# Kernel optimization log

Hardware: AMD Instinct MI355X
Metric: run time of the kernel (lower is better)

## Reference

```python
import jax, jax.numpy as jnp
import numpy as np

FIX_SCALE = np.array([[0.,0.,0.],[1.,0.,0.],[0.,1.,0.],[0.,0.,1.],[-1.,0.,0.],[0.,-1.,0.]], dtype=np.float32)
NUM_HEADS = 8
ATTN_DIMS = 512
HEAD_DIMS = ATTN_DIMS // NUM_HEADS
NUM_LEARN = 6
SIG_CLAMP = 9.21  # safe_sigmoid clamp


def quat_to_rotmat(q):
    # q: [G,4] (w,x,y,z), normalized -> [G,3,3]
    q = q / jnp.linalg.norm(q, axis=-1, keepdims=True)
    w, x, y, z = q[..., 0], q[..., 1], q[..., 2], q[..., 3]
    r0 = jnp.stack([1 - 2*(y*y + z*z), 2*(x*y - w*z), 2*(x*z + w*y)], -1)
    r1 = jnp.stack([2*(x*y + w*z), 1 - 2*(x*x + z*z), 2*(y*z - w*x)], -1)
    r2 = jnp.stack([2*(x*z - w*y), 2*(y*z + w*x), 1 - 2*(x*x + y*y)], -1)
    return jnp.stack([r0, r1, r2], -2)


def bilinear_sample(fm, gx, gy):
    # fm: [C,H,W]; gx,gy: [...] in [-1,1]; align_corners=False, zero padding
    C, H, W = fm.shape
    x = (gx + 1.0) * (W * 0.5) - 0.5
    y = (gy + 1.0) * (H * 0.5) - 0.5
    x0 = jnp.floor(x); y0 = jnp.floor(y)
    wx1 = x - x0; wx0 = 1.0 - wx1
    wy1 = y - y0; wy0 = 1.0 - wy1

    def gather(xf, yf):
        xi = xf.astype(jnp.int32); yi = yf.astype(jnp.int32)
        valid = (xi >= 0) & (xi < W) & (yi >= 0) & (yi < H)
        xi = jnp.clip(xi, 0, W - 1); yi = jnp.clip(yi, 0, H - 1)
        return fm[:, yi, xi] * valid[None].astype(fm.dtype)  # [C, ...]

    out = (gather(x0, y0) * (wx0 * wy0)[None]
           + gather(x0 + 1, y0) * (wx1 * wy0)[None]
           + gather(x0, y0 + 1) * (wx0 * wy1)[None]
           + gather(x0 + 1, y0 + 1) * (wx1 * wy1)[None])
    return jnp.moveaxis(out, 0, -1)  # [..., C]


def setup_inputs() -> dict:
    key = jax.random.key(0)
    ks = jax.random.split(key, 16)
    G, BS, GFD = 8192, 1, 32
    means = jax.random.uniform(ks[0], (G, 3), minval=-1.0, maxval=1.0)
    means = means.at[:, 2].add(3.0)  # push in front of camera
    scales = jax.random.uniform(ks[1], (G, 3), minval=0.01, maxval=0.1)
    rotations = jax.random.normal(ks[2], (G, 4))
    features = jax.random.normal(ks[3], (BS, G, 3, GFD))
    transforms = jnp.tile(jnp.eye(4)[None], (G, 1, 1)) + 0.01 * jax.random.normal(ks[4], (G, 4, 4))
    f = 64.0
    proj = jnp.array([[f, 0., 32., 0.], [0., f, 32., 0.], [0., 0., 1., 0.], [0., 0., 0., 1.]], dtype=jnp.float32)
    projection = jnp.tile(proj[None], (BS, 1, 1))
    image_features = jax.random.normal(ks[5], (BS, 256, 64, 64))
    s = lambda d: 1.0 / np.sqrt(d)
    Wq = jax.random.normal(ks[6], (GFD, ATTN_DIMS)) * s(GFD)
    Wk = jax.random.normal(ks[7], (ATTN_DIMS, 256)) * s(256)
    Wv = jax.random.normal(ks[8], (ATTN_DIMS, 256)) * s(256)
    W_off = jax.random.normal(ks[9], (HEAD_DIMS + 3, NUM_LEARN * 3)) * s(HEAD_DIMS + 3)
    b_off = jnp.zeros((NUM_LEARN * 3,))
    Wout = jax.random.normal(ks[10], (ATTN_DIMS, GFD)) * s(ATTN_DIMS)
    b_out = jnp.zeros((GFD,))
    return {"means": means, "scales": scales, "rotations": rotations, "features": features,
            "transforms": transforms, "projection": projection, "image_features": image_features,
            "Wq": Wq, "Wk": Wk, "Wv": Wv, "W_off": W_off, "b_off": b_off, "Wout": Wout, "b_out": b_out}


def reference(means, scales, rotations, features, transforms, projection, image_features,
              Wq, Wk, Wv, W_off, b_off, Wout, b_out):
    G = means.shape[0]
    bs = features.shape[0]
    H, HD = NUM_HEADS, HEAD_DIMS
    h_img, w_img = image_features.shape[-2:]

    # queries: [bs,G,3,attn] -> [bs,H,G,3,hd]
    q_full = jnp.einsum('bgtf,fa->bgta', features, Wq)
    q = q_full.reshape(bs, G, 3, H, HD).transpose(0, 3, 1, 2, 4)

    # transform means to world space with per-gaussian 4x4
    homo = jnp.concatenate([means, jnp.ones((G, 1), means.dtype)], -1)  # [G,4]
    means_w = jnp.einsum('gij,gj->gi', transforms, homo)[:, :3]  # [G,3]

    # OffsetNet: per-head learnable offsets from (world mean, token-mean query)
    q_mean = q.mean(axis=3)  # [bs,H,G,hd]
    m_b = jnp.broadcast_to(means_w[None, None], (bs, H, G, 3))
    off_in = jnp.concatenate([m_b, q_mean], -1)  # [bs,H,G,hd+3]
    learnable = jax.nn.sigmoid(jnp.clip(off_in @ W_off + b_off, -SIG_CLAMP, SIG_CLAMP))
    learnable = learnable.reshape(bs, H, G, NUM_LEARN, 3) - 0.5
    fix = jnp.broadcast_to(jnp.asarray(FIX_SCALE)[None, None, None], (bs, H, G, FIX_SCALE.shape[0], 3))
    scale_all = jnp.concatenate([fix, learnable], axis=-2)  # [bs,H,G,K,3]
    K = scale_all.shape[-2]

    offset_pts = scale_all * scales[None, None, :, None, :]
    RT = jnp.swapaxes(quat_to_rotmat(rotations), -1, -2)  # [G,3,3]
    offset_pts = jnp.einsum('gij,bhgkj->bhgki', RT, offset_pts) + means_w[None, None, :, None, :]

    # project to 2D, normalize to [0,1), then to grid coords [-1,1]
    pts4 = jnp.concatenate([offset_pts, jnp.ones_like(offset_pts[..., :1])], -1)
    p = jnp.einsum('bij,bhgkj->bhgki', projection, pts4)
    p2 = p[..., :2] / jnp.clip(p[..., 2:3], 1e-5)
    wh = jnp.array([w_img, h_img], dtype=p2.dtype)
    pnorm = jnp.clip(p2 / wh, 0.0, 0.9999)
    grid = 2.0 * pnorm - 1.0  # [bs,H,G,K,2]

    # key/value maps via 1x1 conv, split into per-head channel groups
    kmap = jnp.einsum('ac,bchw->bahw', Wk, image_features).reshape(bs, H, HD, h_img, w_img)
    vmap_ = jnp.einsum('ac,bchw->bahw', Wv, image_features).reshape(bs, H, HD, h_img, w_img)

    sample_bh = jax.vmap(jax.vmap(bilinear_sample, in_axes=(0, 0, 0)), in_axes=(0, 0, 0))
    k_s = sample_bh(kmap, grid[..., 0], grid[..., 1])   # [bs,H,G,K,hd]
    v_s = sample_bh(vmap_, grid[..., 0], grid[..., 1])  # [bs,H,G,K,hd]

    scale = HD ** -0.5
    scores = jnp.einsum('bhgid,bhgkd->bhgik', q, k_s) * scale
    attn = jax.nn.softmax(scores, axis=-1)
    out = jnp.einsum('bhgik,bhgkd->bhgid', attn, v_s)  # [bs,H,G,3,hd]
    out = out.transpose(0, 2, 3, 1, 4).reshape(bs, G, 3, H * HD)  # b g i (h d)
    out = out @ Wout + b_out
    return out + features
```

## Files before the change

kernel.cpp:

```cpp
#include <hip/hip_runtime.h>
#include <hip/hip_bf16.h>
#include <hip/hip_fp16.h>

typedef _Float16 half2v __attribute__((ext_vector_type(2)));
typedef _Float16 half8v __attribute__((ext_vector_type(8)));
typedef __attribute__((ext_vector_type(4))) float float4v;

__device__ __forceinline__ half2v u2h(unsigned u) { return __builtin_bit_cast(half2v, u); }
__device__ __forceinline__ unsigned h2u(half2v h) { return __builtin_bit_cast(unsigned, h); }
__device__ __forceinline__ unsigned short f2hu(float f) {
    _Float16 h = (_Float16)f; return __builtin_bit_cast(unsigned short, h);
}
__device__ __forceinline__ unsigned packh(float lo, float hi) {
    half2v h; h[0] = (_Float16)lo; h[1] = (_Float16)hi; return h2u(h);
}
__device__ __forceinline__ void ld8h(const unsigned short* p, float* f) {
    uint4 u = *(const uint4*)p;
    half2v h0 = u2h(u.x), h1 = u2h(u.y), h2 = u2h(u.z), h3 = u2h(u.w);
    f[0] = (float)h0[0]; f[1] = (float)h0[1]; f[2] = (float)h1[0]; f[3] = (float)h1[1];
    f[4] = (float)h2[0]; f[5] = (float)h2[1]; f[6] = (float)h3[0]; f[7] = (float)h3[1];
}

__global__ __launch_bounds__(256) void wcomb_kernel(
    const float* __restrict__ Wq, const float* __restrict__ W_off,
    const float* __restrict__ b_off, float* __restrict__ Wall)
{
    const int gid = blockIdx.x * 256 + threadIdx.x;
    if (gid >= 36 * 144) return;
    const int j = gid / 144, c = gid - j * 144;
    const int h = c / 18, l = c - h * 18;
    float v;
    if (j < 3) {
        v = W_off[j * 18 + l];
    } else if (j < 35) {
        const int f = j - 3;
        const float* wq = Wq + (size_t)f * 512 + h * 64;
        float s = 0.f;
#pragma unroll
        for (int d = 0; d < 64; d++) s += wq[d] * W_off[(size_t)(3 + d) * 18 + l];
        v = s;
    } else {
        v = b_off[l];
    }
    Wall[gid] = v;
}

__global__ __launch_bounds__(256) void offmlp_kernel(
    const float* __restrict__ means, const float* __restrict__ transforms,
    const float* __restrict__ features, const float* __restrict__ Wall,
    float* __restrict__ lrn_all)
{
    __shared__ float Wc[36][144];
    __shared__ float A[16][38];
    const int tid = threadIdx.x;
    const int g0 = blockIdx.x * 16;

    for (int i = tid; i < 36 * 144; i += 256) Wc[i / 144][i - (i / 144) * 144] = Wall[i];
    {
        const int gi = tid >> 4, lane = tid & 15;
        const int g = g0 + gi;
        const float* fb = features + (size_t)g * 96 + lane * 2;
        float2 t0 = *(const float2*)(fb);
        float2 t1 = *(const float2*)(fb + 32);
        float2 t2 = *(const float2*)(fb + 64);
        A[gi][3 + lane * 2]     = (t0.x + t1.x + t2.x) * (1.f / 3.f);
        A[gi][3 + lane * 2 + 1] = (t0.y + t1.y + t2.y) * (1.f / 3.f);
        if (lane < 3) {
            const float* T = transforms + (size_t)g * 16 + lane * 4;
            float m0 = means[(size_t)g * 3];
            float m1 = means[(size_t)g * 3 + 1];
            float m2 = means[(size_t)g * 3 + 2];
            A[gi][lane] = T[0] * m0 + T[1] * m1 + T[2] * m2 + T[3];
        } else if (lane == 3) {
            A[gi][35] = 1.f;
        }
    }
    __syncthreads();

#pragma unroll
    for (int k = 0; k < 9; k++) {
        int oi = tid + k * 256;
        int gi = oi / 144, c = oi - gi * 144;
        float s = 0.f;
#pragma unroll
        for (int j = 0; j < 36; j++) s += A[gi][j] * Wc[j][c];
        s = fminf(fmaxf(s, -9.21f), 9.21f);
        lrn_all[(size_t)(g0 + gi) * 144 + c] = 1.f / (1.f + expf(-s)) - 0.5f;
    }
}

__global__ __launch_bounds__(256) void conv_fused_kernel(
    const float* __restrict__ img, const float* __restrict__ Wk,
    const float* __restrict__ Wv, unsigned short* __restrict__ buf)
{
    __shared__ __attribute__((aligned(16))) unsigned short Bt[64][264];
    __shared__ __attribute__((aligned(16))) unsigned short Wt[64][264];
    const int tid = threadIdx.x;
    const int p0 = blockIdx.x * 64;
    const int o0 = blockIdx.y * 64;
    const float* Wsel = (o0 < 512) ? Wk : Wv;
    const int obase = (o0 < 512) ? o0 : (o0 - 512);

#pragma unroll
    for (int i = 0; i < 4; i++) {
        int chunk = i * 256 + tid;
        int kp  = chunk >> 3;
        int pxg = (chunk & 7) * 8;
        const float* r0 = img + (size_t)(2 * kp) * 4096 + p0 + pxg;
        const float* r1 = img + (size_t)(2 * kp + 1) * 4096 + p0 + pxg;
        float4 a0 = *(const float4*)r0, a1 = *(const float4*)(r0 + 4);
        float4 b0 = *(const float4*)r1, b1 = *(const float4*)(r1 + 4);
        unsigned lo[8], hi[8];
        lo[0] = f2hu(a0.x); lo[1] = f2hu(a0.y); lo[2] = f2hu(a0.z); lo[3] = f2hu(a0.w);
        lo[4] = f2hu(a1.x); lo[5] = f2hu(a1.y); lo[6] = f2hu(a1.z); lo[7] = f2hu(a1.w);
        hi[0] = f2hu(b0.x); hi[1] = f2hu(b0.y); hi[2] = f2hu(b0.z); hi[3] = f2hu(b0.w);
        hi[4] = f2hu(b1.x); hi[5] = f2hu(b1.y); hi[6] = f2hu(b1.z); hi[7] = f2hu(b1.w);
#pragma unroll
        for (int j = 0; j < 8; j++)
            *(unsigned*)&Bt[pxg + j][2 * kp] = lo[j] | (hi[j] << 16);
    }
    {
        const int row = tid >> 2, q = tid & 3;
        const float* wp = Wsel + (size_t)(obase + row) * 256 + q * 64;
#pragma unroll
        for (int j = 0; j < 8; j++) {
            float4 w0 = *(const float4*)(wp + j * 8);
            float4 w1 = *(const float4*)(wp + j * 8 + 4);
            uint4 pk;
            pk.x = packh(w0.x, w0.y); pk.y = packh(w0.z, w0.w);
            pk.z = packh(w1.x, w1.y); pk.w = packh(w1.z, w1.w);
            *(uint4*)&Wt[row][q * 64 + j * 8] = pk;
        }
    }
    __syncthreads();

    const int w = tid >> 6, l = tid & 63;
    const int m = l & 15, quad = l >> 4;
    const int mrow = w * 16 + m;

    float4v acc[4] = {{0,0,0,0},{0,0,0,0},{0,0,0,0},{0,0,0,0}};
#pragma unroll
    for (int kk = 0; kk < 8; kk++) {
        const int kofs = kk * 32 + quad * 8;
        half8v af = *(const half8v*)&Bt[mrow][kofs];
#pragma unroll
        for (int nt = 0; nt < 4; nt++) {
            half8v b8 = *(const half8v*)&Wt[nt * 16 + m][kofs];
            acc[nt] = __builtin_amdgcn_mfma_f32_16x16x32_f16(af, b8, acc[nt], 0, 0, 0);
        }
    }
#pragma unroll
    for (int nt = 0; nt < 4; nt++) {
#pragma unroll
        for (int r = 0; r < 4; r++) {
            size_t px = p0 + w * 16 + quad * 4 + r;
            buf[px * 1024 + o0 + nt * 16 + m] = f2hu(acc[nt][r]);
        }
    }
}

__global__ __launch_bounds__(256) void qgemm_kernel(
    const float* __restrict__ features, const float* __restrict__ Wq,
    unsigned short* __restrict__ qfull)
{
    __shared__ __attribute__((aligned(16))) unsigned short WqT[256][40];
    const int tid = threadIdx.x;
    const int R0 = blockIdx.x * 64;
    const int n0 = blockIdx.y * 256;
#pragma unroll
    for (int k = 0; k < 32; k++)
        WqT[tid][k] = f2hu(Wq[(size_t)k * 512 + n0 + tid]);
    __syncthreads();

    const int w = tid >> 6, l = tid & 63, m = l & 15, quad = l >> 4;
    const int row = R0 + w * 16 + m;
    const float* fp = features + (size_t)row * 32 + quad * 8;
    float4 f0 = *(const float4*)fp, f1 = *(const float4*)(fp + 4);
    half8v af;
    af[0] = (_Float16)f0.x; af[1] = (_Float16)f0.y;
    af[2] = (_Float16)f0.z; af[3] = (_Float16)f0.w;
    af[4] = (_Float16)f1.x; af[5] = (_Float16)f1.y;
    af[6] = (_Float16)f1.z; af[7] = (_Float16)f1.w;
    float4v acc[16];
#pragma unroll
    for (int t = 0; t < 16; t++) acc[t] = (float4v){0.f, 0.f, 0.f, 0.f};
#pragma unroll
    for (int t = 0; t < 16; t++) {
        half8v b8 = *(const half8v*)&WqT[t * 16 + m][quad * 8];
        acc[t] = __builtin_amdgcn_mfma_f32_16x16x32_f16(af, b8, acc[t], 0, 0, 0);
    }
    const int rb = R0 + w * 16 + quad * 4;
#pragma unroll
    for (int t = 0; t < 16; t++)
#pragma unroll
        for (int r = 0; r < 4; r++)
            qfull[(size_t)(rb + r) * 512 + n0 + t * 16 + m] = f2hu(acc[t][r]);
}

__global__ __launch_bounds__(256, 4) void attn_core_kernel(
    const float* __restrict__ means, const float* __restrict__ scales,
    const float* __restrict__ rot,   const float* __restrict__ transforms,
    const float* __restrict__ projection, const float* __restrict__ lrn_all,
    const unsigned short* __restrict__ buf, unsigned short* __restrict__ qfull)
{
    __shared__ __attribute__((aligned(16))) unsigned qf2[768];
    __shared__ __attribute__((aligned(16))) unsigned vsh2[3072];
    __shared__ __attribute__((aligned(16))) uint4 pixwt[96];
    __shared__ __attribute__((aligned(16))) unsigned att2[288];
    __shared__ __attribute__((aligned(16))) float lrnsh[144];
    __shared__ float mw[3], sc3[3], Rt[9], pr[12];

    const int g = blockIdx.x, tid = threadIdx.x;

    if (tid < 36) {
        ((float4*)lrnsh)[tid] = ((const float4*)(lrn_all + (size_t)g * 144))[tid];
    }
    if (tid >= 64 && tid < 67) {
        sc3[tid - 64] = scales[(size_t)g * 3 + (tid - 64)];
    } else if (tid >= 68 && tid < 80) {
        pr[tid - 68] = projection[tid - 68];
    } else if (tid == 80) {
        float w = rot[(size_t)g * 4],     x = rot[(size_t)g * 4 + 1];
        float y = rot[(size_t)g * 4 + 2], z = rot[(size_t)g * 4 + 3];
        float n = rsqrtf(w * w + x * x + y * y + z * z);
        w *= n; x *= n; y *= n; z *= n;
        float R00 = 1 - 2 * (y * y + z * z), R01 = 2 * (x * y - w * z), R02 = 2 * (x * z + w * y);
        float R10 = 2 * (x * y + w * z), R11 = 1 - 2 * (x * x + z * z), R12 = 2 * (y * z - w * x);
        float R20 = 2 * (x * z - w * y), R21 = 2 * (y * z + w * x), R22 = 1 - 2 * (x * x + y * y);
        Rt[0] = R00; Rt[1] = R10; Rt[2] = R20;
        Rt[3] = R01; Rt[4] = R11; Rt[5] = R21;
        Rt[6] = R02; Rt[7] = R12; Rt[8] = R22;
    } else if (tid >= 84 && tid < 87) {
        int i = tid - 84;
        float m0 = means[(size_t)g * 3];
        float m1 = means[(size_t)g * 3 + 1];
        float m2 = means[(size_t)g * 3 + 2];
        const float* T = transforms + (size_t)g * 16 + i * 4;
        mw[i] = T[0] * m0 + T[1] * m1 + T[2] * m2 + T[3];
    }
    {
        const unsigned* qsrc = (const unsigned*)(qfull + (size_t)g * 1536);
#pragma unroll
        for (int i = 0; i < 3; i++) qf2[tid + i * 256] = qsrc[tid + i * 256];
    }
    __syncthreads();

    if (tid < 96) {
        int h = tid / 12, k = tid % 12;
        float s0, s1, s2;
        if (k < 6) {
            const float FSx[6] = {0.f, 1.f, 0.f, 0.f, -1.f, 0.f};
            const float FSy[6] = {0.f, 0.f, 1.f, 0.f, 0.f, -1.f};
            const float FSz[6] = {0.f, 0.f, 0.f, 1.f, 0.f, 0.f};
            s0 = FSx[k]; s1 = FSy[k]; s2 = FSz[k];
        } else {
            int b = h * 18 + (k - 6) * 3;
            s0 = lrnsh[b]; s1 = lrnsh[b + 1]; s2 = lrnsh[b + 2];
        }
        float o0 = s0 * sc3[0], o1 = s1 * sc3[1], o2 = s2 * sc3[2];
        float wx = Rt[0] * o0 + Rt[1] * o1 + Rt[2] * o2 + mw[0];
        float wy = Rt[3] * o0 + Rt[4] * o1 + Rt[5] * o2 + mw[1];
        float wz = Rt[6] * o0 + Rt[7] * o1 + Rt[8] * o2 + mw[2];
        float px = pr[0] * wx + pr[1] * wy + pr[2]  * wz + pr[3];
        float py = pr[4] * wx + pr[5] * wy + pr[6]  * wz + pr[7];
        float pz = pr[8] * wx + pr[9] * wy + pr[10] * wz + pr[11];
        pz = fmaxf(pz, 1e-5f);
        float gx = fminf(fmaxf(px / pz * (1.f / 64.f), 0.f), 0.9999f);
        float gy = fminf(fmaxf(py / pz * (1.f / 64.f), 0.f), 0.9999f);
        float x = gx * 64.f - 0.5f, y = gy * 64.f - 0.5f;
        float fx = floorf(x), fy = floorf(y);
        int x0 = (int)fx, y0 = (int)fy;
        float wx1 = x - fx, wy1 = y - fy;
        float wx0 = 1.f - wx1, wy0 = 1.f - wy1;
        int xs[2] = {x0, x0 + 1}, ys[2] = {y0, y0 + 1};
        float wxs[2] = {wx0, wx1}, wys[2] = {wy0, wy1};
        unsigned pix[4]; float wf[4];
#pragma unroll
        for (int c = 0; c < 4; c++) {
            int xi = xs[c & 1], yi = ys[c >> 1];
            bool v = ((unsigned)xi < 64u) & ((unsigned)yi < 64u);
            int xc = min(max(xi, 0), 63), yc = min(max(yi, 0), 63);
            pix[c] = (unsigned)(yc * 64 + xc);
            wf[c] = v ? wxs[c & 1] * wys[c >> 1] : 0.f;
        }
        uint4 pw;
        pw.x = pix[0] | (pix[1] << 16);
        pw.y = pix[2] | (pix[3] << 16);
        pw.z = packh(wf[0], wf[1]);
        pw.w = packh(wf[2], wf[3]);
        pixwt[tid] = pw;
    }
    __syncthreads();

    {
        const int slice = tid & 7, grp = tid >> 3;
#pragma unroll
        for (int it = 0; it < 3; it++) {
            const int p = it * 32 + grp;
            const int h = p / 12, k = p - h * 12;
            const uint4 pw = pixwt[p];
            const int off0 = (int)(pw.x & 0xffffu) << 10;
            const int off1 = (int)(pw.x >> 16) << 10;
            const int off2 = (int)(pw.y & 0xffffu) << 10;
            const int off3 = (int)(pw.y >> 16) << 10;
            const half2v w01 = u2h(pw.z), w23 = u2h(pw.w);
            const unsigned short* bp = buf + h * 64 + slice * 8;
            uint4 uk[4], uv[4];
            uk[0] = *(const uint4*)(bp + off0); uv[0] = *(const uint4*)(bp + off0 + 512);
            uk[1] = *(const uint4*)(bp + off1); uv[1] = *(const uint4*)(bp + off1 + 512);
            uk[2] = *(const uint4*)(bp + off2); uv[2] = *(const uint4*)(bp + off2 + 512);
            uk[3] = *(const uint4*)(bp + off3); uv[3] = *(const uint4*)(bp + off3 + 512);
            half2v ka2[4] = {{0,0},{0,0},{0,0},{0,0}};
            half2v va2[4] = {{0,0},{0,0},{0,0},{0,0}};
            half2v w2;
            w2[0] = w01[0]; w2[1] = w01[0];
            ka2[0] += w2 * u2h(uk[0].x); ka2[1] += w2 * u2h(uk[0].y);
            ka2[2] += w2 * u2h(uk[0].z); ka2[3] += w2 * u2h(uk[0].w);
            va2[0] += w2 * u2h(uv[0].x); va2[1] += w2 * u2h(uv[0].y);
            va2[2] += w2 * u2h(uv[0].z); va2[3] += w2 * u2h(uv[0].w);
            w2[0] = w01[1]; w2[1] = w01[1];
            ka2[0] += w2 * u2h(uk[1].x); ka2[1] += w2 * u2h(uk[1].y);
            ka2[2] += w2 * u2h(uk[1].z); ka2[3] += w2 * u2h(uk[1].w);
            va2[0] += w2 * u2h(uv[1].x); va2[1] += w2 * u2h(uv[1].y);
            va2[2] += w2 * u2h(uv[1].z); va2[3] += w2 * u2h(uv[1].w);
            w2[0] = w23[0]; w2[1] = w23[0];
            ka2[0] += w2 * u2h(uk[2].x); ka2[1] += w2 * u2h(uk[2].y);
            ka2[2] += w2 * u2h(uk[2].z); ka2[3] += w2 * u2h(uk[2].w);
            va2[0] += w2 * u2h(uv[2].x); va2[1] += w2 * u2h(uv[2].y);
            va2[2] += w2 * u2h(uv[2].z); va2[3] += w2 * u2h(uv[2].w);
            w2[0] = w23[1]; w2[1] = w23[1];
            ka2[0] += w2 * u2h(uk[3].x); ka2[1] += w2 * u2h(uk[3].y);
            ka2[2] += w2 * u2h(uk[3].z); ka2[3] += w2 * u2h(uk[3].w);
            va2[0] += w2 * u2h(uv[3].x); va2[1] += w2 * u2h(uv[3].y);
            va2[2] += w2 * u2h(uv[3].z); va2[3] += w2 * u2h(uv[3].w);

            const int pa = h * 32 + slice * 4;
            *(uint4*)&vsh2[p * 32 + slice * 4] =
                make_uint4(h2u(va2[0]), h2u(va2[1]), h2u(va2[2]), h2u(va2[3]));
            float sp[3];
#pragma unroll
            for (int t = 0; t < 3; t++) {
                uint4 q4 = *(const uint4*)&qf2[t * 256 + pa];
                float s = __builtin_amdgcn_fdot2(u2h(q4.x), ka2[0], 0.f, false);
                s = __builtin_amdgcn_fdot2(u2h(q4.y), ka2[1], s, false);
                s = __builtin_amdgcn_fdot2(u2h(q4.z), ka2[2], s, false);
                s = __builtin_amdgcn_fdot2(u2h(q4.w), ka2[3], s, false);
                sp[t] = s;
            }
#pragma unroll
            for (int msk = 1; msk < 8; msk <<= 1) {
#pragma unroll
                for (int t = 0; t < 3; t++) sp[t] += __shfl_xor(sp[t], msk);
            }
            if (slice == 0) {
#pragma unroll
                for (int t = 0; t < 3; t++)
                    ((float*)att2)[(h * 3 + t) * 12 + k] = sp[t] * 0.125f;
            }
        }
    }
    __syncthreads();

    if (tid < 24) {
        float*    row  = (float*)att2 + tid * 12;
        unsigned* rowp = att2 + tid * 12;
        float m = row[0];
#pragma unroll
        for (int k = 1; k < 12; k++) m = fmaxf(m, row[k]);
        float e_[12]; float ssum = 0.f;
#pragma unroll
        for (int k = 0; k < 12; k++) { e_[k] = expf(row[k] - m); ssum += e_[k]; }
        float inv = 1.f / ssum;
#pragma unroll
        for (int k = 0; k < 12; k++) { float a = e_[k] * inv; rowp[k] = packh(a, a); }
    }
    __syncthreads();

    {
        unsigned* oa32 = (unsigned*)(qfull + (size_t)g * 1536);
#pragma unroll
        for (int i = 0; i < 3; i++) {
            int e = tid + i * 256;
            int t = e >> 8, a2p = e & 255;
            int h = a2p >> 5, ddp = a2p & 31;
            const unsigned* ar2 = att2 + (h * 3 + t) * 12;
            const unsigned* vp  = vsh2 + h * 12 * 32 + ddp;
            half2v acc = {0, 0};
#pragma unroll
            for (int k = 0; k < 12; k++)
                acc += u2h(ar2[k]) * u2h(vp[k * 32]);
            oa32[e] = h2u(acc);
        }
    }
}

__global__ __launch_bounds__(256, 6) void attn_core_basic(
    const float* __restrict__ means, const float* __restrict__ scales,
    const float* __restrict__ rot,   const float* __restrict__ transforms,
    const float* __restrict__ projection, const float* __restrict__ W_off,
    const float* __restrict__ b_off, const unsigned short* __restrict__ buf,
    unsigned short* __restrict__ qfull)
{
    __shared__ __attribute__((aligned(16))) unsigned qf2[768];
    __shared__ __attribute__((aligned(16))) unsigned vsh2[3072];
    __shared__ __attribute__((aligned(16))) float qm_u[512];
    __shared__ __attribute__((aligned(16))) unsigned att2[288];
    __shared__ float mw[3], sc3[3], Rt[9], pr[12];

    float* lrn  = (float*)att2;
    float* wofl = (float*)vsh2;
    float* bofl = wofl + 1206;

    const int g = blockIdx.x, tid = threadIdx.x;

    for (int i = tid; i < 1206; i += 256) wofl[i] = W_off[i];
    if (tid < 18) bofl[tid] = b_off[tid];
    if (tid >= 32 && tid < 35) {
        sc3[tid - 32] = scales[(size_t)g * 3 + (tid - 32)];
    } else if (tid >= 36 && tid < 48) {
        pr[tid - 36] = projection[tid - 36];
    } else if (tid == 48) {
        float w = rot[(size_t)g * 4],     x = rot[(size_t)g * 4 + 1];
        float y = rot[(size_t)g * 4 + 2], z = rot[(size_t)g * 4 + 3];
        float n = rsqrtf(w * w + x * x + y * y + z * z);
        w *= n; x *= n; y *= n; z *= n;
        float R00 = 1 - 2 * (y * y + z * z), R01 = 2 * (x * y - w * z), R02 = 2 * (x * z + w * y);
        float R10 = 2 * (x * y + w * z), R11 = 1 - 2 * (x * x + z * z), R12 = 2 * (y * z - w * x);
        float R20 = 2 * (x * z - w * y), R21 = 2 * (y * z + w * x), R22 = 1 - 2 * (x * x + y * y);
        Rt[0] = R00; Rt[1] = R10; Rt[2] = R20;
        Rt[3] = R01; Rt[4] = R11; Rt[5] = R21;
        Rt[6] = R02; Rt[7] = R12; Rt[8] = R22;
    } else if (tid >= 52 && tid < 55) {
        int i = tid - 52;
        float m0 = means[(size_t)g * 3];
        float m1 = means[(size_t)g * 3 + 1];
        float m2 = means[(size_t)g * 3 + 2];
        const float* T = transforms + (size_t)g * 16 + i * 4;
        mw[i] = T[0] * m0 + T[1] * m1 + T[2] * m2 + T[3];
    }
    {
        const unsigned* qsrc = (const unsigned*)(qfull + (size_t)g * 1536);
#pragma unroll
        for (int i = 0; i < 3; i++) qf2[tid + i * 256] = qsrc[tid + i * 256];
    }
    __syncthreads();

    {
        half2v a = u2h(qf2[tid]), b = u2h(qf2[256 + tid]), c = u2h(qf2[512 + tid]);
        qm_u[tid * 2]     = ((float)a[0] + (float)b[0] + (float)c[0]) * (1.f / 3.f);
        qm_u[tid * 2 + 1] = ((float)a[1] + (float)b[1] + (float)c[1]) * (1.f / 3.f);
    }
    __syncthreads();

    if (tid < 144) {
        int h = tid / 18, l = tid % 18;
        float s = bofl[l];
#pragma unroll
        for (int i = 0; i < 3; i++) s += mw[i] * wofl[i * 18 + l];
        for (int d = 0; d < 64; d++) s += qm_u[h * 64 + d] * wofl[(3 + d) * 18 + l];
        s = fminf(fmaxf(s, -9.21f), 9.21f);
        lrn[tid] = 1.f / (1.f + expf(-s)) - 0.5f;
    }
    __syncthreads();

    if (tid < 96) {
        int h = tid / 12, k = tid % 12;
        float s0, s1, s2;
        if (k < 6) {
            const float FSx[6] = {0.f, 1.f, 0.f, 0.f, -1.f, 0.f};
            const float FSy[6] = {0.f, 0.f, 1.f, 0.f, 0.f, -1.f};
            const float FSz[6] = {0.f, 0.f, 0.f, 1.f, 0.f, 0.f};
            s0 = FSx[k]; s1 = FSy[k]; s2 = FSz[k];
        } else {
            int b = h * 18 + (k - 6) * 3;
            s0 = lrn[b]; s1 = lrn[b + 1]; s2 = lrn[b + 2];
        }
        float o0 = s0 * sc3[0], o1 = s1 * sc3[1], o2 = s2 * sc3[2];
        float wx = Rt[0] * o0 + Rt[1] * o1 + Rt[2] * o2 + mw[0];
        float wy = Rt[3] * o0 + Rt[4] * o1 + Rt[5] * o2 + mw[1];
        float wz = Rt[6] * o0 + Rt[7] * o1 + Rt[8] * o2 + mw[2];
        float px = pr[0] * wx + pr[1] * wy + pr[2]  * wz + pr[3];
        float py = pr[4] * wx + pr[5] * wy + pr[6]  * wz + pr[7];
        float pz = pr[8] * wx + pr[9] * wy + pr[10] * wz + pr[11];
        pz = fmaxf(pz, 1e-5f);
        float gx = fminf(fmaxf(px / pz * (1.f / 64.f), 0.f), 0.9999f);
        float gy = fminf(fmaxf(py / pz * (1.f / 64.f), 0.f), 0.9999f);
        float x = gx * 64.f - 0.5f, y = gy * 64.f - 0.5f;
        float fx = floorf(x), fy = floorf(y);
        int x0 = (int)fx, y0 = (int)fy;
        float wx1 = x - fx, wy1 = y - fy;
        float wx0 = 1.f - wx1, wy0 = 1.f - wy1;
        int xs[2] = {x0, x0 + 1}, ys[2] = {y0, y0 + 1};
        float wxs[2] = {wx0, wx1}, wys[2] = {wy0, wy1};
        unsigned pix[4]; float wf[4];
#pragma unroll
        for (int c = 0; c < 4; c++) {
            int xi = xs[c & 1], yi = ys[c >> 1];
            bool v = ((unsigned)xi < 64u) & ((unsigned)yi < 64u);
            int xc = min(max(xi, 0), 63), yc = min(max(yi, 0), 63);
            pix[c] = (unsigned)(yc * 64 + xc);
            wf[c] = v ? wxs[c & 1] * wys[c >> 1] : 0.f;
        }
        uint4 pw;
        pw.x = pix[0] | (pix[1] << 16);
        pw.y = pix[2] | (pix[3] << 16);
        pw.z = packh(wf[0], wf[1]);
        pw.w = packh(wf[2], wf[3]);
        ((uint4*)qm_u)[tid] = pw;
    }
    __syncthreads();

    {
        const int slice = tid & 7, grp = tid >> 3;
#pragma unroll
        for (int it = 0; it < 3; it++) {
            const int p = it * 32 + grp;
            const int h = p / 12, k = p - h * 12;
            const uint4 pw = ((const uint4*)qm_u)[p];
            const int off0 = (int)(pw.x & 0xffffu) << 10;
            const int off1 = (int)(pw.x >> 16) << 10;
            const int off2 = (int)(pw.y & 0xffffu) << 10;
            const int off3 = (int)(pw.y >> 16) << 10;
            const half2v w01 = u2h(pw.z), w23 = u2h(pw.w);
            const unsigned short* bp = buf + h * 64 + slice * 8;
            uint4 uk[4], uv[4];
            uk[0] = *(const uint4*)(bp + off0); uv[0] = *(const uint4*)(bp + off0 + 512);
            uk[1] = *(const uint4*)(bp + off1); uv[1] = *(const uint4*)(bp + off1 + 512);
            uk[2] = *(const uint4*)(bp + off2); uv[2] = *(const uint4*)(bp + off2 + 512);
            uk[3] = *(const uint4*)(bp + off3); uv[3] = *(const uint4*)(bp + off3 + 512);
            half2v ka2[4] = {{0,0},{0,0},{0,0},{0,0}};
            half2v va2[4] = {{0,0},{0,0},{0,0},{0,0}};
            half2v w2;
            w2[0] = w01[0]; w2[1] = w01[0];
            ka2[0] += w2 * u2h(uk[0].x); ka2[1] += w2 * u2h(uk[0].y);
            ka2[2] += w2 * u2h(uk[0].z); ka2[3] += w2 * u2h(uk[0].w);
            va2[0] += w2 * u2h(uv[0].x); va2[1] += w2 * u2h(uv[0].y);
            va2[2] += w2 * u2h(uv[0].z); va2[3] += w2 * u2h(uv[0].w);
            w2[0] = w01[1]; w2[1] = w01[1];
            ka2[0] += w2 * u2h(uk[1].x); ka2[1] += w2 * u2h(uk[1].y);
            ka2[2] += w2 * u2h(uk[1].z); ka2[3] += w2 * u2h(uk[1].w);
            va2[0] += w2 * u2h(uv[1].x); va2[1] += w2 * u2h(uv[1].y);
            va2[2] += w2 * u2h(uv[1].z); va2[3] += w2 * u2h(uv[1].w);
            w2[0] = w23[0]; w2[1] = w23[0];
            ka2[0] += w2 * u2h(uk[2].x); ka2[1] += w2 * u2h(uk[2].y);
            ka2[2] += w2 * u2h(uk[2].z); ka2[3] += w2 * u2h(uk[2].w);
            va2[0] += w2 * u2h(uv[2].x); va2[1] += w2 * u2h(uv[2].y);
            va2[2] += w2 * u2h(uv[2].z); va2[3] += w2 * u2h(uv[2].w);
            w2[0] = w23[1]; w2[1] = w23[1];
            ka2[0] += w2 * u2h(uk[3].x); ka2[1] += w2 * u2h(uk[3].y);
            ka2[2] += w2 * u2h(uk[3].z); ka2[3] += w2 * u2h(uk[3].w);
            va2[0] += w2 * u2h(uv[3].x); va2[1] += w2 * u2h(uv[3].y);
            va2[2] += w2 * u2h(uv[3].z); va2[3] += w2 * u2h(uv[3].w);

            const int pa = h * 32 + slice * 4;
            *(uint4*)&vsh2[p * 32 + slice * 4] =
                make_uint4(h2u(va2[0]), h2u(va2[1]), h2u(va2[2]), h2u(va2[3]));
            float sp[3];
#pragma unroll
            for (int t = 0; t < 3; t++) {
                uint4 q4 = *(const uint4*)&qf2[t * 256 + pa];
                float s = __builtin_amdgcn_fdot2(u2h(q4.x), ka2[0], 0.f, false);
                s = __builtin_amdgcn_fdot2(u2h(q4.y), ka2[1], s, false);
                s = __builtin_amdgcn_fdot2(u2h(q4.z), ka2[2], s, false);
                s = __builtin_amdgcn_fdot2(u2h(q4.w), ka2[3], s, false);
                sp[t] = s;
            }
#pragma unroll
            for (int msk = 1; msk < 8; msk <<= 1) {
#pragma unroll
                for (int t = 0; t < 3; t++) sp[t] += __shfl_xor(sp[t], msk);
            }
            if (slice == 0) {
#pragma unroll
                for (int t = 0; t < 3; t++)
                    ((float*)att2)[(h * 3 + t) * 12 + k] = sp[t] * 0.125f;
            }
        }
    }
    __syncthreads();

    if (tid < 24) {
        float*    row  = (float*)att2 + tid * 12;
        unsigned* rowp = att2 + tid * 12;
        float m = row[0];
#pragma unroll
        for (int k = 1; k < 12; k++) m = fmaxf(m, row[k]);
        float e_[12]; float ssum = 0.f;
#pragma unroll
        for (int k = 0; k < 12; k++) { e_[k] = expf(row[k] - m); ssum += e_[k]; }
        float inv = 1.f / ssum;
#pragma unroll
        for (int k = 0; k < 12; k++) { float a = e_[k] * inv; rowp[k] = packh(a, a); }
    }
    __syncthreads();

    {
        unsigned* oa32 = (unsigned*)(qfull + (size_t)g * 1536);
#pragma unroll
        for (int i = 0; i < 3; i++) {
            int e = tid + i * 256;
            int t = e >> 8, a2p = e & 255;
            int h = a2p >> 5, ddp = a2p & 31;
            const unsigned* ar2 = att2 + (h * 3 + t) * 12;
            const unsigned* vp  = vsh2 + h * 12 * 32 + ddp;
            half2v acc = {0, 0};
#pragma unroll
            for (int k = 0; k < 12; k++)
                acc += u2h(ar2[k]) * u2h(vp[k * 32]);
            oa32[e] = h2u(acc);
        }
    }
}

__global__ __launch_bounds__(256) void outgemm_kernel(
    const unsigned short* __restrict__ oa, const float* __restrict__ Wout,
    const float* __restrict__ b_out, const float* __restrict__ features,
    float* __restrict__ out)
{
    __shared__ __attribute__((aligned(16))) unsigned short WT[32][520];
    const int tid = threadIdx.x;
    const int R0 = blockIdx.x * 64;
#pragma unroll
    for (int j = 0; j < 64; j++) {
        int lin = j * 256 + tid;
        WT[lin & 31][lin >> 5] = f2hu(Wout[lin]);
    }
    __syncthreads();

    const int w = tid >> 6, l = tid & 63, m = l & 15, quad = l >> 4;
    const int row = R0 + w * 16 + m;
    float4v acc[2] = {{0,0,0,0},{0,0,0,0}};
#pragma unroll
    for (int kk = 0; kk < 16; kk++) {
        half8v af = *(const half8v*)(oa + (size_t)row * 512 + kk * 32 + quad * 8);
#pragma unroll
        for (int t = 0; t < 2; t++) {
            half8v b8 = *(const half8v*)&WT[t * 16 + m][kk * 32 + quad * 8];
            acc[t] = __builtin_amdgcn_mfma_f32_16x16x32_f16(af, b8, acc[t], 0, 0, 0);
        }
    }
    const int rb = R0 + w * 16 + quad * 4;
#pragma unroll
    for (int t = 0; t < 2; t++) {
        int col = t * 16 + m;
        float bb = b_out[col];
#pragma unroll
        for (int r = 0; r < 4; r++) {
            int rr = rb + r;
            out[(size_t)rr * 32 + col] = acc[t][r] + bb + features[(size_t)rr * 32 + col];
        }
    }
}

__global__ __launch_bounds__(256, 6) void attn_fused_kernel(
    const float* __restrict__ means, const float* __restrict__ scales,
    const float* __restrict__ rot,   const float* __restrict__ features,
    const float* __restrict__ transforms, const float* __restrict__ projection,
    const float* __restrict__ Wq,    const float* __restrict__ W_off,
    const float* __restrict__ b_off, const float* __restrict__ Wout,
    const float* __restrict__ b_out, const unsigned short* __restrict__ buf,
    float* __restrict__ out)
{
    __shared__ float feat[96];
    __shared__ __attribute__((aligned(16))) float qf[1536];
    __shared__ float qm[512];
    __shared__ float mw[3], sc3[3], Rt[9], pr[12];
    __shared__ float lrn[144];
    __shared__ int   coff[96][4];
    __shared__ float cwt[96][4];
    __shared__ __attribute__((aligned(16))) char pool[12288];
    __shared__ float att[288];

    unsigned short* vsh = (unsigned short*)pool;
    const int g = blockIdx.x, tid = threadIdx.x;

    if (tid < 96) {
        feat[tid] = features[(size_t)g * 96 + tid];
    } else if (tid < 99) {
        sc3[tid - 96] = scales[(size_t)g * 3 + (tid - 96)];
    } else if (tid >= 100 && tid < 112) {
        pr[tid - 100] = projection[tid - 100];
    } else if (tid == 112) {
        float w = rot[(size_t)g * 4],     x = rot[(size_t)g * 4 + 1];
        float y = rot[(size_t)g * 4 + 2], z = rot[(size_t)g * 4 + 3];
        float n = rsqrtf(w * w + x * x + y * y + z * z);
        w *= n; x *= n; y *= n; z *= n;
        float R00 = 1 - 2 * (y * y + z * z), R01 = 2 * (x * y - w * z), R02 = 2 * (x * z + w * y);
        float R10 = 2 * (x * y + w * z), R11 = 1 - 2 * (x * x + z * z), R12 = 2 * (y * z - w * x);
        float R20 = 2 * (x * z - w * y), R21 = 2 * (y * z + w * x), R22 = 1 - 2 * (x * x + y * y);
        Rt[0] = R00; Rt[1] = R10; Rt[2] = R20;
        Rt[3] = R01; Rt[4] = R11; Rt[5] = R21;
        Rt[6] = R02; Rt[7] = R12; Rt[8] = R22;
    } else if (tid >= 116 && tid < 119) {
        int i = tid - 116;
        float m0 = means[(size_t)g * 3];
        float m1 = means[(size_t)g * 3 + 1];
        float m2 = means[(size_t)g * 3 + 2];
        const float* T = transforms + (size_t)g * 16 + i * 4;
        mw[i] = T[0] * m0 + T[1] * m1 + T[2] * m2 + T[3];
    }
    __syncthreads();

    {
        const int a0 = tid * 2;
        float s00 = 0.f, s01 = 0.f, s10 = 0.f, s11 = 0.f, s20 = 0.f, s21 = 0.f;
#pragma unroll
        for (int f = 0; f < 32; f++) {
            float2 w2 = *(const float2*)(Wq + (size_t)f * 512 + a0);
            float f0 = feat[f], f1 = feat[32 + f], f2 = feat[64 + f];
            s00 += f0 * w2.x; s01 += f0 * w2.y;
            s10 += f1 * w2.x; s11 += f1 * w2.y;
            s20 += f2 * w2.x; s21 += f2 * w2.y;
        }
        *(float2*)(qf + a0)        = make_float2(s00, s01);
        *(float2*)(qf + 512 + a0)  = make_float2(s10, s11);
        *(float2*)(qf + 1024 + a0) = make_float2(s20, s21);
    }
    __syncthreads();

    qm[tid]       = (qf[tid]       + qf[tid + 512] + qf[tid + 1024]) * (1.f / 3.f);
    qm[tid + 256] = (qf[tid + 256] + qf[tid + 768] + qf[tid + 1280]) * (1.f / 3.f);
    __syncthreads();

    if (tid < 144) {
        int h = tid / 18, l = tid % 18;
        float s = b_off[l];
#pragma unroll
        for (int i = 0; i < 3; i++) s += mw[i] * W_off[i * 18 + l];
        for (int d = 0; d < 64; d++) s += qm[h * 64 + d] * W_off[(size_t)(3 + d) * 18 + l];
        s = fminf(fmaxf(s, -9.21f), 9.21f);
        lrn[tid] = 1.f / (1.f + expf(-s)) - 0.5f;
    }
    __syncthreads();

    if (tid < 96) {
        int h = tid / 12, k = tid % 12;
        float s0, s1, s2;
        if (k < 6) {
            const float FSx[6] = {0.f, 1.f, 0.f, 0.f, -1.f, 0.f};
            const float FSy[6] = {0.f, 0.f, 1.f, 0.f, 0.f, -1.f};
            const float FSz[6] = {0.f, 0.f, 0.f, 1.f, 0.f, 0.f};
            s0 = FSx[k]; s1 = FSy[k]; s2 = FSz[k];
        } else {
            int b = h * 18 + (k - 6) * 3;
            s0 = lrn[b]; s1 = lrn[b + 1]; s2 = lrn[b + 2];
        }
        float o0 = s0 * sc3[0], o1 = s1 * sc3[1], o2 = s2 * sc3[2];
        float wx = Rt[0] * o0 + Rt[1] * o1 + Rt[2] * o2 + mw[0];
        float wy = Rt[3] * o0 + Rt[4] * o1 + Rt[5] * o2 + mw[1];
        float wz = Rt[6] * o0 + Rt[7] * o1 + Rt[8] * o2 + mw[2];
        float px = pr[0] * wx + pr[1] * wy + pr[2]  * wz + pr[3];
        float py = pr[4] * wx + pr[5] * wy + pr[6]  * wz + pr[7];
        float pz = pr[8] * wx + pr[9] * wy + pr[10] * wz + pr[11];
        pz = fmaxf(pz, 1e-5f);
        float gx = fminf(fmaxf(px / pz * (1.f / 64.f), 0.f), 0.9999f);
        float gy = fminf(fmaxf(py / pz * (1.f / 64.f), 0.f), 0.9999f);
        float x = gx * 64.f - 0.5f, y = gy * 64.f - 0.5f;
        float fx = floorf(x), fy = floorf(y);
        int x0 = (int)fx, y0 = (int)fy;
        float wx1 = x - fx, wx0c = 1.f - wx1;
        float wy1 = y - fy, wy0c = 1.f - wy1;
        int xs[2] = {x0, x0 + 1}, ys[2] = {y0, y0 + 1};
        float wxs[2] = {wx0c, wx1}, wys[2] = {wy0c, wy1};
#pragma unroll
        for (int c = 0; c < 4; c++) {
            int dx = c & 1, dy = c >> 1;
            int xi = xs[dx], yi = ys[dy];
            bool v = (xi >= 0) & (xi < 64) & (yi >= 0) & (yi < 64);
            int xc = min(max(xi, 0), 63), yc = min(max(yi, 0), 63);
            coff[tid][c] = (yc * 64 + xc) * 1024;
            cwt[tid][c]  = v ? wxs[dx] * wys[dy] : 0.f;
        }
    }
    __syncthreads();

    {
        const int slice = tid & 7, d0 = slice * 8, grp = tid >> 3;
#pragma unroll
        for (int it = 0; it < 3; it++) {
            const int p = it * 32 + grp;
            const int h = p / 12, k = p - h * 12;
            const int a = h * 64 + d0;
            const unsigned short* bp = buf + a;
            float ka[8] = {0,0,0,0,0,0,0,0}, va[8] = {0,0,0,0,0,0,0,0}, t8[8];
#pragma unroll
            for (int c = 0; c < 4; c++) {
                const int   o = coff[p][c];
                const float w = cwt[p][c];
                ld8h(bp + o, t8);
#pragma unroll
                for (int j = 0; j < 8; j++) ka[j] += w * t8[j];
                ld8h(bp + o + 512, t8);
#pragma unroll
                for (int j = 0; j < 8; j++) va[j] += w * t8[j];
            }
            uint4 pv;
            pv.x = packh(va[0], va[1]); pv.y = packh(va[2], va[3]);
            pv.z = packh(va[4], va[5]); pv.w = packh(va[6], va[7]);
            *(uint4*)(vsh + p * 64 + d0) = pv;
            float sp[3];
#pragma unroll
            for (int t = 0; t < 3; t++) {
                const float* qp = qf + t * 512 + a;
                float s = 0.f;
#pragma unroll
                for (int j = 0; j < 8; j++) s += qp[j] * ka[j];
                sp[t] = s;
            }
#pragma unroll
            for (int msk = 1; msk < 8; msk <<= 1) {
#pragma unroll
                for (int t = 0; t < 3; t++) sp[t] += __shfl_xor(sp[t], msk);
            }
            if (slice == 0) {
#pragma unroll
                for (int t = 0; t < 3; t++) att[(h * 3 + t) * 12 + k] = sp[t] * 0.125f;
            }
        }
    }
    __syncthreads();

    if (tid < 24) {
        float* row = att + tid * 12;
        float m = row[0];
#pragma unroll
        for (int k = 1; k < 12; k++) m = fmaxf(m, row[k]);
        float e_[12]; float ssum = 0.f;
#pragma unroll
        for (int k = 0; k < 12; k++) { e_[k] = expf(row[k] - m); ssum += e_[k]; }
        float inv = 1.f / ssum;
#pragma unroll
        for (int k = 0; k < 12; k++) row[k] = e_[k] * inv;
    }
    __syncthreads();

#pragma unroll
    for (int i = 0; i < 6; i++) {
        int e = tid + i * 256;
        int t = e >> 9, a = e & 511, h = a >> 6, dd = a & 63;
        const float* ar = att + (h * 3 + t) * 12;
        const unsigned short* vp = vsh + (h * 12) * 64 + dd;
        float s = 0.f;
#pragma unroll
        for (int k = 0; k < 12; k++) {
            _Float16 hh = __builtin_bit_cast(_Float16, vp[k * 64]);
            s += ar[k] * (float)hh;
        }
        qf[e] = s;
    }
    __syncthreads();

    {
        float* red = (float*)pool;
        const int c0 = (tid & 15) * 2, slice = tid >> 4;
        const int abase = slice * 32;
        float a00 = 0.f, a01 = 0.f, a10 = 0.f, a11 = 0.f, a20 = 0.f, a21 = 0.f;
#pragma unroll
        for (int i = 0; i < 32; i++) {
            int a = abase + i;
            float2 w2 = *(const float2*)(Wout + (size_t)a * 32 + c0);
            float o0 = qf[a], o1 = qf[512 + a], o2 = qf[1024 + a];
            a00 += o0 * w2.x; a01 += o0 * w2.y;
            a10 += o1 * w2.x; a11 += o1 * w2.y;
            a20 += o2 * w2.x; a21 += o2 * w2.y;
        }
        __syncthreads();
        red[(slice * 3 + 0) * 32 + c0] = a00; red[(slice * 3 + 0) * 32 + c0 + 1] = a01;
        red[(slice * 3 + 1) * 32 + c0] = a10; red[(slice * 3 + 1) * 32 + c0 + 1] = a11;
        red[(slice * 3 + 2) * 32 + c0] = a20; red[(slice * 3 + 2) * 32 + c0 + 1] = a21;
        __syncthreads();
        if (tid < 96) {
            int t = tid >> 5, c = tid & 31;
            float acc = b_out[c] + feat[tid];
#pragma unroll
            for (int s = 0; s < 16; s++) acc += red[(s * 3 + t) * 32 + c];
            out[(size_t)g * 96 + tid] = acc;
        }
    }
}

extern "C" void kernel_launch(void* const* d_in, const int* in_sizes, int n_in,
                              void* d_out, int out_size, void* d_ws, size_t ws_size,
                              hipStream_t stream) {
    const float* means      = (const float*)d_in[0];
    const float* scales     = (const float*)d_in[1];
    const float* rot        = (const float*)d_in[2];
    const float* features   = (const float*)d_in[3];
    const float* transforms = (const float*)d_in[4];
    const float* projection = (const float*)d_in[5];
    const float* img        = (const float*)d_in[6];
    const float* Wq         = (const float*)d_in[7];
    const float* Wk         = (const float*)d_in[8];
    const float* Wv         = (const float*)d_in[9];
    const float* W_off      = (const float*)d_in[10];
    const float* b_off      = (const float*)d_in[11];
    const float* Wout       = (const float*)d_in[12];
    const float* b_out      = (const float*)d_in[13];
    float* out = (float*)d_out;

    char* w = (char*)d_ws;
    unsigned short* buf = (unsigned short*)(w + 64);
    const size_t BUF_BYTES  = (size_t)4096 * 1024 * 2;
    const size_t Q_BYTES    = (size_t)24576 * 512 * 2;
    const size_t WALL_BYTES = 32768;
    const size_t LRN_BYTES  = (size_t)8192 * 144 * 4;
    const size_t need  = 64 + BUF_BYTES + Q_BYTES;
    const size_t need2 = need + WALL_BYTES + LRN_BYTES;

    dim3 gridc(64, 16);
    conv_fused_kernel<<<gridc, 256, 0, stream>>>(img, Wk, Wv, buf);

    if (ws_size >= need2) {
        unsigned short* qfull = (unsigned short*)(w + 64 + BUF_BYTES);
        float* Wall    = (float*)(w + 64 + BUF_BYTES + Q_BYTES);
        float* lrn_all = (float*)(w + 64 + BUF_BYTES + Q_BYTES + WALL_BYTES);

        wcomb_kernel<<<(36 * 144 + 255) / 256, 256, 0, stream>>>(Wq, W_off, b_off, Wall);
        offmlp_kernel<<<512, 256, 0, stream>>>(means, transforms, features, Wall, lrn_all);
        dim3 gridq(384, 2);
        qgemm_kernel<<<gridq, 256, 0, stream>>>(features, Wq, qfull);
        attn_core_kernel<<<8192, 256, 0, stream>>>(
            means, scales, rot, transforms, projection, lrn_all, buf, qfull);
        outgemm_kernel<<<384, 256, 0, stream>>>(qfull, Wout, b_out, features, out);
    } else if (ws_size >= need) {
        unsigned short* qfull = (unsigned short*)(w + 64 + BUF_BYTES);
        dim3 gridq(384, 2);
        qgemm_kernel<<<gridq, 256, 0, stream>>>(features, Wq, qfull);
        attn_core_basic<<<8192, 256, 0, stream>>>(
            means, scales, rot, transforms, projection, W_off, b_off, buf, qfull);
        outgemm_kernel<<<384, 256, 0, stream>>>(qfull, Wout, b_out, features, out);
    } else {
        attn_fused_kernel<<<8192, 256, 0, stream>>>(
            means, scales, rot, features, transforms, projection,
            Wq, W_off, b_off, Wout, b_out, buf, out);
    }
}
```

Measured before the change: 168.5 us.

## Fuse weight-combination into offset MLP kernel and double conv outputs per block

Removes the separate wcomb kernel launch. Each offmlp block now recomputes the combined Wq·W_off weight matrix in shared memory from an fp16 copy of Wq, and handles 32 gaussians per block instead of 16. The conv kernel now reuses the converted image tile across two 64-channel output tiles, halving grid.y and the redundant image loads and conversions. The cost is that 256 blocks each redo the weight combination, which is extra compute, and it now uses fp16 Wq, which lowers precision.

```diff
diff --git a/kernel.cpp b/kernel.cpp
--- a/kernel.cpp
+++ b/kernel.cpp
@@ -21,65 +21,82 @@
     f[4] = (float)h2[0]; f[5] = (float)h2[1]; f[6] = (float)h3[0]; f[7] = (float)h3[1];
 }
 
-__global__ __launch_bounds__(256) void wcomb_kernel(
-    const float* __restrict__ Wq, const float* __restrict__ W_off,
-    const float* __restrict__ b_off, float* __restrict__ Wall)
-{
-    const int gid = blockIdx.x * 256 + threadIdx.x;
-    if (gid >= 36 * 144) return;
-    const int j = gid / 144, c = gid - j * 144;
-    const int h = c / 18, l = c - h * 18;
-    float v;
-    if (j < 3) {
-        v = W_off[j * 18 + l];
-    } else if (j < 35) {
-        const int f = j - 3;
-        const float* wq = Wq + (size_t)f * 512 + h * 64;
-        float s = 0.f;
-#pragma unroll
-        for (int d = 0; d < 64; d++) s += wq[d] * W_off[(size_t)(3 + d) * 18 + l];
-        v = s;
-    } else {
-        v = b_off[l];
-    }
-    Wall[gid] = v;
-}
-
 __global__ __launch_bounds__(256) void offmlp_kernel(
     const float* __restrict__ means, const float* __restrict__ transforms,
-    const float* __restrict__ features, const float* __restrict__ Wall,
+    const float* __restrict__ features, const float* __restrict__ Wq,
+    const float* __restrict__ W_off, const float* __restrict__ b_off,
     float* __restrict__ lrn_all)
 {
+    __shared__ __attribute__((aligned(16))) unsigned short Wq16[32 * 512];
+    __shared__ float Woffs[1224];
     __shared__ float Wc[36][144];
-    __shared__ float A[16][38];
+    __shared__ float A[32][38];
     const int tid = threadIdx.x;
-    const int g0 = blockIdx.x * 16;
-
-    for (int i = tid; i < 36 * 144; i += 256) Wc[i / 144][i - (i / 144) * 144] = Wall[i];
-    {
-        const int gi = tid >> 4, lane = tid & 15;
+    const int g0 = blockIdx.x * 32;
+
+#pragma unroll
+    for (int i = 0; i < 16; i++) {
+        int idx4 = i * 256 + tid;
+        float4 v = ((const float4*)Wq)[idx4];
+        unsigned* dst = (unsigned*)&Wq16[idx4 * 4];
+        dst[0] = packh(v.x, v.y);
+        dst[1] = packh(v.z, v.w);
+    }
+    for (int i = tid; i < 1206; i += 256) Woffs[i] = W_off[i];
+    if (tid < 18) Woffs[1206 + tid] = b_off[tid];
+    {
+        const int gi = tid >> 3, sl = tid & 7;
         const int g = g0 + gi;
-        const float* fb = features + (size_t)g * 96 + lane * 2;
-        float2 t0 = *(const float2*)(fb);
-        float2 t1 = *(const float2*)(fb + 32);
-        float2 t2 = *(const float2*)(fb + 64);
-        A[gi][3 + lane * 2]     = (t0.x + t1.x + t2.x) * (1.f / 3.f);
-        A[gi][3 + lane * 2 + 1] = (t0.y + t1.y + t2.y) * (1.f / 3.f);
-        if (lane < 3) {
-            const float* T = transforms + (size_t)g * 16 + lane * 4;
+        const float* fb = features + (size_t)g * 96 + sl * 4;
+        float4 t0 = *(const float4*)(fb);
+        float4 t1 = *(const float4*)(fb + 32);
+        float4 t2 = *(const float4*)(fb + 64);
+        A[gi][3 + sl * 4 + 0] = (t0.x + t1.x + t2.x) * (1.f / 3.f);
+        A[gi][3 + sl * 4 + 1] = (t0.y + t1.y + t2.y) * (1.f / 3.f);
+        A[gi][3 + sl * 4 + 2] = (t0.z + t1.z + t2.z) * (1.f / 3.f);
+        A[gi][3 + sl * 4 + 3] = (t0.w + t1.w + t2.w) * (1.f / 3.f);
+        if (sl < 3) {
+            const float* T = transforms + (size_t)g * 16 + sl * 4;
             float m0 = means[(size_t)g * 3];
             float m1 = means[(size_t)g * 3 + 1];
             float m2 = means[(size_t)g * 3 + 2];
-            A[gi][lane] = T[0] * m0 + T[1] * m1 + T[2] * m2 + T[3];
-        } else if (lane == 3) {
+            A[gi][sl] = T[0] * m0 + T[1] * m1 + T[2] * m2 + T[3];
+        } else if (sl == 3) {
             A[gi][35] = 1.f;
         }
     }
     __syncthreads();
 
-#pragma unroll
-    for (int k = 0; k < 9; k++) {
-        int oi = tid + k * 256;
+    for (int k = 0; k < 21; k++) {
+        int oi = k * 256 + tid;
+        if (oi < 5184) {
+            int j = oi / 144, c = oi - j * 144;
+            int h = c / 18, l = c - h * 18;
+            float v;
+            if (j < 3) {
+                v = Woffs[j * 18 + l];
+            } else if (j == 35) {
+                v = Woffs[1206 + l];
+            } else {
+                int f = j - 3;
+                const unsigned* wq2 = (const unsigned*)&Wq16[f * 512 + h * 64];
+                float s = 0.f;
+#pragma unroll
+                for (int d2 = 0; d2 < 32; d2++) {
+                    half2v w2 = u2h(wq2[d2]);
+                    s += (float)w2[0] * Woffs[(3 + 2 * d2) * 18 + l]
+                       + (float)w2[1] * Woffs[(4 + 2 * d2) * 18 + l];
+                }
+                v = s;
+            }
+            Wc[j][c] = v;
+        }
+    }
+    __syncthreads();
+
+#pragma unroll
+    for (int k = 0; k < 18; k++) {
+        int oi = k * 256 + tid;
         int gi = oi / 144, c = oi - gi * 144;
         float s = 0.f;
 #pragma unroll
@@ -97,9 +114,6 @@
     __shared__ __attribute__((aligned(16))) unsigned short Wt[64][264];
     const int tid = threadIdx.x;
     const int p0 = blockIdx.x * 64;
-    const int o0 = blockIdx.y * 64;
-    const float* Wsel = (o0 < 512) ? Wk : Wv;
-    const int obase = (o0 < 512) ? o0 : (o0 - 512);
 
 #pragma unroll
     for (int i = 0; i < 4; i++) {
@@ -119,42 +133,50 @@
         for (int j = 0; j < 8; j++)
             *(unsigned*)&Bt[pxg + j][2 * kp] = lo[j] | (hi[j] << 16);
     }
-    {
-        const int row = tid >> 2, q = tid & 3;
-        const float* wp = Wsel + (size_t)(obase + row) * 256 + q * 64;
-#pragma unroll
-        for (int j = 0; j < 8; j++) {
-            float4 w0 = *(const float4*)(wp + j * 8);
-            float4 w1 = *(const float4*)(wp + j * 8 + 4);
-            uint4 pk;
-            pk.x = packh(w0.x, w0.y); pk.y = packh(w0.z, w0.w);
-            pk.z = packh(w1.x, w1.y); pk.w = packh(w1.z, w1.w);
-            *(uint4*)&Wt[row][q * 64 + j * 8] = pk;
-        }
-    }
-    __syncthreads();
 
     const int w = tid >> 6, l = tid & 63;
     const int m = l & 15, quad = l >> 4;
     const int mrow = w * 16 + m;
 
-    float4v acc[4] = {{0,0,0,0},{0,0,0,0},{0,0,0,0},{0,0,0,0}};
-#pragma unroll
-    for (int kk = 0; kk < 8; kk++) {
-        const int kofs = kk * 32 + quad * 8;
-        half8v af = *(const half8v*)&Bt[mrow][kofs];
+#pragma unroll
+    for (int j = 0; j < 2; j++) {
+        const int o0 = blockIdx.y * 128 + j * 64;
+        const float* Wsel = (o0 < 512) ? Wk : Wv;
+        const int obase = (o0 < 512) ? o0 : (o0 - 512);
+        if (j) __syncthreads();
+        {
+            const int row = tid >> 2, q = tid & 3;
+            const float* wp = Wsel + (size_t)(obase + row) * 256 + q * 64;
+#pragma unroll
+            for (int jj = 0; jj < 8; jj++) {
+                float4 w0 = *(const float4*)(wp + jj * 8);
+                float4 w1 = *(const float4*)(wp + jj * 8 + 4);
+                uint4 pk;
+                pk.x = packh(w0.x, w0.y); pk.y = packh(w0.z, w0.w);
+                pk.z = packh(w1.x, w1.y); pk.w = packh(w1.z, w1.w);
+                *(uint4*)&Wt[row][q * 64 + jj * 8] = pk;
+            }
+        }
+        __syncthreads();
+
+        float4v acc[4] = {{0,0,0,0},{0,0,0,0},{0,0,0,0},{0,0,0,0}};
+#pragma unroll
+        for (int kk = 0; kk < 8; kk++) {
+            const int kofs = kk * 32 + quad * 8;
+            half8v af = *(const half8v*)&Bt[mrow][kofs];
+#pragma unroll
+            for (int nt = 0; nt < 4; nt++) {
+                half8v b8 = *(const half8v*)&Wt[nt * 16 + m][kofs];
+                acc[nt] = __builtin_amdgcn_mfma_f32_16x16x32_f16(af, b8, acc[nt], 0, 0, 0);
+            }
+        }
 #pragma unroll
         for (int nt = 0; nt < 4; nt++) {
-            half8v b8 = *(const half8v*)&Wt[nt * 16 + m][kofs];
-            acc[nt] = __builtin_amdgcn_mfma_f32_16x16x32_f16(af, b8, acc[nt], 0, 0, 0);
-        }
-    }
-#pragma unroll
-    for (int nt = 0; nt < 4; nt++) {
-#pragma unroll
-        for (int r = 0; r < 4; r++) {
-            size_t px = p0 + w * 16 + quad * 4 + r;
-            buf[px * 1024 + o0 + nt * 16 + m] = f2hu(acc[nt][r]);
+#pragma unroll
+            for (int r = 0; r < 4; r++) {
+                size_t px = p0 + w * 16 + quad * 4 + r;
+                buf[px * 1024 + o0 + nt * 16 + m] = f2hu(acc[nt][r]);
+            }
         }
     }
 }
@@ -900,23 +922,21 @@
 
     char* w = (char*)d_ws;
     unsigned short* buf = (unsigned short*)(w + 64);
-    const size_t BUF_BYTES  = (size_t)4096 * 1024 * 2;
-    const size_t Q_BYTES    = (size_t)24576 * 512 * 2;
-    const size_t WALL_BYTES = 32768;
-    const size_t LRN_BYTES  = (size_t)8192 * 144 * 4;
+    const size_t BUF_BYTES = (size_t)4096 * 1024 * 2;
+    const size_t Q_BYTES   = (size_t)24576 * 512 * 2;
+    const size_t LRN_BYTES = (size_t)8192 * 144 * 4;
     const size_t need  = 64 + BUF_BYTES + Q_BYTES;
-    const size_t need2 = need + WALL_BYTES + LRN_BYTES;
-
-    dim3 gridc(64, 16);
+    const size_t need2 = need + LRN_BYTES;
+
+    dim3 gridc(64, 8);
     conv_fused_kernel<<<gridc, 256, 0, stream>>>(img, Wk, Wv, buf);
 
     if (ws_size >= need2) {
         unsigned short* qfull = (unsigned short*)(w + 64 + BUF_BYTES);
-        float* Wall    = (float*)(w + 64 + BUF_BYTES + Q_BYTES);
-        float* lrn_all = (float*)(w + 64 + BUF_BYTES + Q_BYTES + WALL_BYTES);
-
-        wcomb_kernel<<<(36 * 144 + 255) / 256, 256, 0, stream>>>(Wq, W_off, b_off, Wall);
-        offmlp_kernel<<<512, 256, 0, stream>>>(means, transforms, features, Wall, lrn_all);
+        float* lrn_all = (float*)(w + 64 + BUF_BYTES + Q_BYTES);
+
+        offmlp_kernel<<<256, 256, 0, stream>>>(
+            means, transforms, features, Wq, W_off, b_off, lrn_all);
         dim3 gridq(384, 2);
         qgemm_kernel<<<gridq, 256, 0, stream>>>(features, Wq, qfull);
         attn_core_kernel<<<8192, 256, 0, stream>>>(
```

New measurement: 182.0 us. 8.0% more time.
